# Performance work log

Hardware: AMD Instinct MI355X
Metric: run time of the kernel (lower is better)

## Reference

```python
import jax, jax.numpy as jnp
import numpy as np

BITS = 4
MAXQ = (1 << BITS) - 1      # 15
PACK = 32 // BITS           # 8 values per int32 word
GROUP = 128                 # quantization group size along K


def setup_inputs() -> dict:
    key = jax.random.key(0)
    k0, k1, k2, k3 = jax.random.split(key, 4)
    M, K, N = 4096, 4096, 11008
    G = K // GROUP
    x = jax.random.normal(k0, (M, K), dtype=jnp.float32)
    # packed 4-bit weights: full-range random int32 words (each holds 8 nibbles)
    qweight = jax.random.randint(k1, (K // PACK, N), -(2**31), 2**31 - 1, dtype=jnp.int32)
    # packed zero points: (G, N // PACK) int32 words
    qzeros = jax.random.randint(k2, (G, N // PACK), -(2**31), 2**31 - 1, dtype=jnp.int32)
    # group-wise scales (G, N), small positive values as GPTQ produces
    scales = jax.random.uniform(k3, (G, N), dtype=jnp.float32, minval=1e-3, maxval=1e-2)
    # standard GPTQ grouping: consecutive blocks of GROUP rows share a group
    g_idx = (jnp.arange(K) // GROUP).astype(jnp.int32)
    return {"x": x, "qweight": qweight, "scales": scales, "qzeros": qzeros, "g_idx": g_idx}


def _dequant(qweight, scales, qzeros, g_idx):
    """Unpack int32-packed 4-bit weights and dequantize to float. Returns (K, N)."""
    K = g_idx.shape[0]
    N = qweight.shape[1]
    k = jnp.arange(K)
    # nibble k lives in word k//PACK at bit offset (k%PACK)*BITS
    k_shift = ((k % PACK) * BITS).astype(jnp.int32)
    w = (qweight[k // PACK] >> k_shift[:, None]) & MAXQ              # (K, N) int32 in [0, MAXQ]
    n = jnp.arange(N)
    n_shift = ((n % PACK) * BITS).astype(jnp.int32)
    z = ((qzeros[:, n // PACK] >> n_shift[None, :]) & MAXQ) + 1      # (G, N); kernel adds 1
    return (w - z[g_idx]).astype(scales.dtype) * scales[g_idx]       # (K, N) float


def reference(x, qweight, scales, qzeros, g_idx):
    # C = A @ dequant(B), fp32 accumulation as in the Triton kernel
    W = _dequant(qweight, scales, qzeros, g_idx)
    return jnp.matmul(x, W, preferred_element_type=jnp.float32)
```

## Files before the change

### kernel.cpp

```cpp
#include <hip/hip_runtime.h>
#include <hip/hip_bf16.h>
#include <stdint.h>

typedef _Float16 half8 __attribute__((ext_vector_type(8)));
typedef __attribute__((ext_vector_type(8))) short short8;
typedef __attribute__((ext_vector_type(4))) float floatx4;
typedef __attribute__((ext_vector_type(4))) uint32_t uint32x4;

#define GROUP_SZ 128

__device__ __forceinline__ uint32_t cvt_pk_f16(float lo, float hi) {
    uint32_t r;
    asm("v_cvt_pkrtz_f16_f32 %0, %1, %2" : "=v"(r) : "v"(lo), "v"(hi));
    return r;
}
__device__ __forceinline__ uint32_t pk_add_f16(uint32_t a, uint32_t b) {
    uint32_t r;
    asm("v_pk_add_f16 %0, %1, %2" : "=v"(r) : "v"(a), "v"(b));
    return r;
}
__device__ __forceinline__ uint32_t pk_mul_f16(uint32_t a, uint32_t b) {
    uint32_t r;
    asm("v_pk_mul_f16 %0, %1, %2" : "=v"(r) : "v"(a), "v"(b));
    return r;
}

__global__ __launch_bounds__(256)
void convA_kernel(const float* __restrict__ x, uint4* __restrict__ aws, int total8) {
    int idx = blockIdx.x * 256 + threadIdx.x;
    if (idx >= total8) return;
    const float4* xp = reinterpret_cast<const float4*>(x) + (size_t)idx * 2;
    float4 a = xp[0], b = xp[1];
    uint4 o;
    o.x = cvt_pk_f16(a.x, a.y);
    o.y = cvt_pk_f16(a.z, a.w);
    o.z = cvt_pk_f16(b.x, b.y);
    o.w = cvt_pk_f16(b.z, b.w);
    aws[idx] = o;
}

__global__ __launch_bounds__(256)
void deqB_kernel(const int* __restrict__ qw, const float* __restrict__ sc,
                 const int* __restrict__ qz, char* __restrict__ bws, int K, int N) {
    const int n = blockIdx.x * 256 + threadIdx.x;
    const int wk = blockIdx.y;
    if (n >= N) return;
    const uint32_t w = (uint32_t)qw[(size_t)wk * N + n];
    const int g = wk >> 4;
    const float s = sc[(size_t)g * N + n];
    const uint32_t zw = (uint32_t)qz[(size_t)g * (N >> 3) + (n >> 3)];
    const float zf = -(float)(1025u + ((zw >> ((n & 7) * 4)) & 15u));
    const uint32_t c2 = cvt_pk_f16(zf, zf);
    const uint32_t s2 = cvt_pk_f16(s, s);
    uint32_t oo[4];
    #pragma unroll
    for (int i = 0; i < 4; ++i) {
        const uint32_t tt = w >> (8 * i);
        const uint32_t qi = ((tt & 0xFu) | 0x64006400u) | ((tt << 12) & 0xF0000u);
        oo[i] = pk_mul_f16(pk_add_f16(qi, c2), s2);
    }
    uint4 o; o.x = oo[0]; o.y = oo[1]; o.z = oo[2]; o.w = oo[3];
    const int NKT = K >> 6;
    const int nt = n >> 8, h = (n >> 7) & 1, row = n & 127;
    const int kt = wk >> 3, slot = wk & 7;
    size_t off = ((((size_t)nt * NKT + kt) * 2 + h) * 8 + slot) * 2048 + (size_t)row * 16;
    *reinterpret_cast<uint4*>(bws + off) = o;
}

__global__ __launch_bounds__(512, 2)
void gemm8_kernel(const char* __restrict__ Aws, const char* __restrict__ Bws,
                  float* __restrict__ out, int M, int K, int N) {
    __shared__ char smem[65536];

    const int NT = K >> 6;
    const int nbm = M >> 8, nbn = N >> 8;
    const int nwg = nbm * nbn;
    int bid = blockIdx.x;
    int q = nwg >> 3, r = nwg & 7;
    int xcd = bid & 7, lin = bid >> 3;
    int sid = (xcd < r ? xcd * (q + 1) : r * (q + 1) + (xcd - r) * q) + lin;
    const int bm = sid % nbm, bn = sid / nbm;
    const int m0 = bm << 8, n0 = bn << 8;

    const int tid = threadIdx.x;
    const int lane = tid & 63, w = tid >> 6;
    const int wm = w >> 2, wn = w & 3;
    const int fr = lane & 15, hi = lane >> 4;
    const int r8 = lane >> 3, c8 = lane & 7;

    const uint32_t K2 = (uint32_t)K * 2;
    const char* aBase = Aws + (size_t)m0 * K2;
    uint32_t aOff[2][2];
    #pragma unroll
    for (int h = 0; h < 2; ++h)
        #pragma unroll
        for (int i = 0; i < 2; ++i)
            aOff[h][i] = (uint32_t)(h * 128 + w * 16 + i * 8 + r8) * K2
                       + (uint32_t)((c8 ^ r8) * 16);
    const char* bBase = Bws + (size_t)bn * ((size_t)NT * 32768);

    auto stageA = [&](uint32_t buf, int kt) {
        #pragma unroll
        for (int h = 0; h < 2; ++h)
            #pragma unroll
            for (int i = 0; i < 2; ++i) {
                const char* src = aBase + aOff[h][i] + (uint32_t)kt * 128u;
                char* dst = smem + buf * 32768u + (uint32_t)h * 16384u
                                 + (uint32_t)w * 2048u + (uint32_t)i * 1024u;
                __builtin_amdgcn_global_load_lds(
                    (const __attribute__((address_space(1))) void*)src,
                    (__attribute__((address_space(3))) void*)dst, 16, 0, 0);
            }
    };

    floatx4 acc[8][4];
    const floatx4 fz = {0.f, 0.f, 0.f, 0.f};
    #pragma unroll
    for (int i = 0; i < 8; ++i)
        #pragma unroll
        for (int j = 0; j < 4; ++j) acc[i][j] = fz;
    half8 af_a[4][2], af_b[4][2];
    half8 bf_x[2][2], bf_y[2][2];

#define LOAD_AF(AF, QM) { _Pragma("unroll") for (int fmi = 0; fmi < 4; ++fmi) { \
    _Pragma("unroll") for (int kk = 0; kk < 2; ++kk) { \
        uint32_t row = (uint32_t)(wm * 128 + ((QM) * 4 + fmi) * 16 + fr); \
        uint32_t p = (uint32_t)((kk * 4 + hi) ^ (fr & 7)); \
        uint32x4 u = *reinterpret_cast<const uint32x4*>(As + row * 128u + p * 16u); \
        AF[fmi][kk] = __builtin_bit_cast(half8, u); } } }

#define LOAD_BFG(BF, QN, KT) { _Pragma("unroll") for (int fnj = 0; fnj < 2; ++fnj) { \
    _Pragma("unroll") for (int kk = 0; kk < 2; ++kk) { \
        uint32_t nl = (uint32_t)(wn * 64 + ((QN) * 2 + fnj) * 16 + fr); \
        uint32_t slot = (uint32_t)(kk * 4 + hi); \
        size_t off = ((size_t)((KT) * 2 + (int)(nl >> 7)) * 8 + slot) * 2048 \
                   + (size_t)(nl & 127u) * 16u; \
        uint32x4 u = *reinterpret_cast<const uint32x4*>(bBase + off); \
        BF[fnj][kk] = __builtin_bit_cast(half8, u); } } }

#define MM(AF, BF, QM, QN) { _Pragma("unroll") for (int kk = 0; kk < 2; ++kk) \
    _Pragma("unroll") for (int fmi = 0; fmi < 4; ++fmi) \
    _Pragma("unroll") for (int fnj = 0; fnj < 2; ++fnj) \
        acc[(QM) * 4 + fmi][(QN) * 2 + fnj] = __builtin_amdgcn_mfma_f32_16x16x32_f16( \
            AF[fmi][kk], BF[fnj][kk], acc[(QM) * 4 + fmi][(QN) * 2 + fnj], 0, 0, 0); }

    stageA(0, 0);
    if (NT > 1) stageA(1, 1);
    LOAD_BFG(bf_x, 0, 0);
    LOAD_BFG(bf_y, 1, 0);
    if (NT > 1) { asm volatile("s_waitcnt vmcnt(12)" ::: "memory"); }
    else        { asm volatile("s_waitcnt vmcnt(8)" ::: "memory"); }
    __builtin_amdgcn_s_barrier();

    for (int t = 0; t < NT; ++t) {
        const uint32_t c = (uint32_t)(t & 1);
        const char* As = smem + c * 32768u;
        const bool st1 = (t + 1 < NT);
        const bool st2 = (t + 2 < NT);
        LOAD_AF(af_a, 0);
        LOAD_AF(af_b, 1);
        __builtin_amdgcn_s_setprio(1);
        MM(af_a, bf_x, 0, 0);
        MM(af_b, bf_x, 1, 0);
        __builtin_amdgcn_s_setprio(0);
        if (st1) LOAD_BFG(bf_x, 0, t + 1);
        __builtin_amdgcn_s_setprio(1);
        MM(af_a, bf_y, 0, 1);
        MM(af_b, bf_y, 1, 1);
        __builtin_amdgcn_s_setprio(0);
        if (st1) LOAD_BFG(bf_y, 1, t + 1);
        __builtin_amdgcn_s_barrier();
        if (st2) {
            stageA(c, t + 2);
            asm volatile("s_waitcnt vmcnt(12)" ::: "memory");
        } else if (st1) {
            asm volatile("s_waitcnt vmcnt(8)" ::: "memory");
        }
        if (st1) __builtin_amdgcn_s_barrier();
    }
#undef LOAD_AF
#undef LOAD_BFG
#undef MM

    float* op = out + (size_t)(m0 + wm * 128) * N + n0 + wn * 64;
    #pragma unroll
    for (int fm = 0; fm < 8; ++fm)
        #pragma unroll
        for (int fn = 0; fn < 4; ++fn)
            #pragma unroll
            for (int rr = 0; rr < 4; ++rr)
                op[(size_t)(fm * 16 + hi * 4 + rr) * N + fn * 16 + fr] = acc[fm][fn][rr];
}

__device__ __forceinline__ uint32_t cvt_pk_bf16(float lo, float hi) {
    uint32_t r;
    asm("v_cvt_pk_bf16_f32 %0, %1, %2" : "=v"(r) : "v"(lo), "v"(hi));
    return r;
}
__device__ __forceinline__ uint32_t fswz(uint32_t row, uint32_t byte_in_row) {
    return row * 128u + (byte_in_row ^ ((row & 7u) << 4));
}

__global__ __launch_bounds__(256, 2)
void fused128_kernel(const float* __restrict__ x, const int* __restrict__ qweight,
                     const float* __restrict__ scales, const int* __restrict__ qzeros,
                     float* __restrict__ out, int M, int K, int N) {
    __shared__ char smem[32768];
    char* Ald = smem;
    char* Bld = smem + 16384;
    const int nbm = M / 128, nbn = N / 128;
    const int nwg = nbm * nbn;
    int bid = blockIdx.x;
    int q = nwg >> 3, r = nwg & 7;
    int xcd = bid & 7, lin = bid >> 3;
    int sid = (xcd < r ? xcd * (q + 1) : r * (q + 1) + (xcd - r) * q) + lin;
    int bm = sid / nbn, bn = sid % nbn;
    const int m0 = bm * 128, n0 = bn * 128;
    const int t = threadIdx.x;
    const int lane = t & 63, wave = t >> 6;
    const int tm = t >> 4, tk4 = t & 15;
    const int sn = t & 127, kwh = t >> 7;
    const int gn = n0 + sn;
    const int NT = K / 64;
    float4 av[8]; uint32_t qw[4]; float sc; uint32_t zw;
    const float* xp = x + (size_t)(m0 + tm) * K + tk4 * 4;
    const int* qp = qweight + (size_t)(kwh * 4) * N + gn;
    auto load_tile = [&](int ts) {
        const int k0 = ts * 64;
        #pragma unroll
        for (int i = 0; i < 8; ++i)
            av[i] = *reinterpret_cast<const float4*>(xp + (size_t)i * 16 * K + k0);
        const int g = k0 >> 7;
        sc = scales[(size_t)g * N + gn];
        zw = (uint32_t)qzeros[(size_t)g * (N >> 3) + (gn >> 3)];
        const int* qb = qp + (size_t)(k0 >> 3) * N;
        #pragma unroll
        for (int j = 0; j < 4; ++j) qw[j] = (uint32_t)qb[(size_t)j * N];
    };
    const int zsh = (gn & 7) * 4;
    auto write_tile = [&]() {
        #pragma unroll
        for (int i = 0; i < 8; ++i) {
            uint2 p;
            p.x = cvt_pk_bf16(av[i].x, av[i].y);
            p.y = cvt_pk_bf16(av[i].z, av[i].w);
            *reinterpret_cast<uint2*>(Ald + fswz((uint32_t)(i * 16 + tm), (uint32_t)(tk4 * 8))) = p;
        }
        const float z = (float)((zw >> zsh) & 15u) + 1.0f;
        const float nz = -z * sc;
        #pragma unroll
        for (int j = 0; j < 4; ++j) {
            const uint32_t wv = qw[j];
            float f[8];
            #pragma unroll
            for (int e = 0; e < 8; ++e)
                f[e] = fmaf((float)((wv >> (4 * e)) & 15u), sc, nz);
            uint4 p;
            p.x = cvt_pk_bf16(f[0], f[1]); p.y = cvt_pk_bf16(f[2], f[3]);
            p.z = cvt_pk_bf16(f[4], f[5]); p.w = cvt_pk_bf16(f[6], f[7]);
            *reinterpret_cast<uint4*>(Bld + fswz((uint32_t)sn, (uint32_t)((kwh * 4 + j) * 16))) = p;
        }
    };
    floatx4 acc[4][4];
    const floatx4 fz = {0.f, 0.f, 0.f, 0.f};
    #pragma unroll
    for (int i = 0; i < 4; ++i)
        #pragma unroll
        for (int j = 0; j < 4; ++j) acc[i][j] = fz;
    const int wm = (wave >> 1) * 64, wn = (wave & 1) * 64;
    const int fr = lane & 15;
    const int fkb = ((lane >> 4) * 8) * 2;
    auto compute = [&]() {
        #pragma unroll
        for (int kk = 0; kk < 2; ++kk) {
            short8 afv[4], bfv[4];
            #pragma unroll
            for (int i = 0; i < 4; ++i)
                afv[i] = *reinterpret_cast<const short8*>(
                    Ald + fswz((uint32_t)(wm + i * 16 + fr), (uint32_t)(kk * 64 + fkb)));
            #pragma unroll
            for (int i = 0; i < 4; ++i)
                bfv[i] = *reinterpret_cast<const short8*>(
                    Bld + fswz((uint32_t)(wn + i * 16 + fr), (uint32_t)(kk * 64 + fkb)));
            #pragma unroll
            for (int i = 0; i < 4; ++i)
                #pragma unroll
                for (int j = 0; j < 4; ++j)
                    acc[i][j] = __builtin_amdgcn_mfma_f32_16x16x32_bf16(afv[i], bfv[j], acc[i][j], 0, 0, 0);
        }
    };
    load_tile(0);
    write_tile();
    __syncthreads();
    for (int ts = 0; ts < NT; ++ts) {
        if (ts + 1 < NT) load_tile(ts + 1);
        compute();
        __syncthreads();
        if (ts + 1 < NT) write_tile();
        __syncthreads();
    }
    const int fq = lane >> 4;
    float* op = out + (size_t)(m0 + wm) * N + n0 + wn;
    #pragma unroll
    for (int i = 0; i < 4; ++i)
        #pragma unroll
        for (int j = 0; j < 4; ++j)
            #pragma unroll
            for (int rr = 0; rr < 4; ++rr)
                op[(size_t)(i * 16 + fq * 4 + rr) * N + j * 16 + fr] = acc[i][j][rr];
}

extern "C" void kernel_launch(void* const* d_in, const int* in_sizes, int n_in,
                              void* d_out, int out_size, void* d_ws, size_t ws_size,
                              hipStream_t stream) {
    const float* x       = (const float*)d_in[0];
    const int*   qweight = (const int*)d_in[1];
    const float* scales  = (const float*)d_in[2];
    const int*   qzeros  = (const int*)d_in[3];

    const int K = in_sizes[4];
    const int M = in_sizes[0] / K;
    const int G = K / GROUP_SZ;
    const int N = in_sizes[2] / G;
    float* out = (float*)d_out;

    const size_t needA = (size_t)M * K * 2;
    const size_t needB = (size_t)K * (size_t)N * 2;
    const bool ok = (ws_size >= needA + needB) && (M % 256 == 0) && (N % 256 == 0)
                    && (K % 128 == 0) && (N % 8 == 0);
    if (ok) {
        char* aws = (char*)d_ws;
        char* bws = aws + needA;
        const int total8 = M * (K / 8);
        hipLaunchKernelGGL(convA_kernel, dim3((total8 + 255) / 256), dim3(256), 0, stream,
                           x, (uint4*)aws, total8);
        hipLaunchKernelGGL(deqB_kernel, dim3((N + 255) / 256, K / 8), dim3(256), 0, stream,
                           qweight, scales, qzeros, bws, K, N);
        hipLaunchKernelGGL(gemm8_kernel, dim3((M / 256) * (N / 256)), dim3(512), 0, stream,
                           aws, bws, out, M, K, N);
    } else {
        const int nwg = (M / 128) * (N / 128);
        hipLaunchKernelGGL(fused128_kernel, dim3(nwg), dim3(256), 0, stream,
                           x, qweight, scales, qzeros, out, M, K, N);
    }
}
```

Before: 388.0 us.

## Pre-tile A into MFMA fragment layout and load operands directly to registers

The A conversion kernel now writes fp16 activations in a tiled layout matching the 16x32 MFMA fragment order, so each lane can fetch its fragment with one contiguous 16-byte global load. The GEMM drops LDS staging, async global-to-LDS copies and all barriers, and instead double-buffers A and B fragments in registers straight from global memory. This removes LDS traffic and synchronisation. The cost is that A reuse across the four N-waves now relies on L2/L1 cache rather than shared memory, which raises global load volume and register pressure.

```diff
diff --git a/kernel.cpp b/kernel.cpp
--- a/kernel.cpp
+++ b/kernel.cpp
@@ -26,17 +26,23 @@
 }
 
 __global__ __launch_bounds__(256)
-void convA_kernel(const float* __restrict__ x, uint4* __restrict__ aws, int total8) {
+void convA_kernel(const float* __restrict__ x, char* __restrict__ aws,
+                  int M, int K) {
+    const int KC = K >> 3;
     int idx = blockIdx.x * 256 + threadIdx.x;
-    if (idx >= total8) return;
-    const float4* xp = reinterpret_cast<const float4*>(x) + (size_t)idx * 2;
+    if (idx >= M * KC) return;
+    const int m = idx / KC, c = idx % KC;
+    const float4* xp = reinterpret_cast<const float4*>(x + (size_t)m * K + c * 8);
     float4 a = xp[0], b = xp[1];
     uint4 o;
     o.x = cvt_pk_f16(a.x, a.y);
     o.y = cvt_pk_f16(a.z, a.w);
     o.z = cvt_pk_f16(b.x, b.y);
     o.w = cvt_pk_f16(b.z, b.w);
-    aws[idx] = o;
+    const int kt = c >> 3, slot = c & 7;
+    size_t off = (((size_t)(m >> 4) * (size_t)(K >> 6) + (size_t)kt) * 8 + (size_t)slot) * 256
+               + (size_t)(m & 15) * 16;
+    *reinterpret_cast<uint4*>(aws + off) = o;
 }
 
 __global__ __launch_bounds__(256)
@@ -68,10 +74,8 @@
 }
 
 __global__ __launch_bounds__(512, 2)
-void gemm8_kernel(const char* __restrict__ Aws, const char* __restrict__ Bws,
-                  float* __restrict__ out, int M, int K, int N) {
-    __shared__ char smem[65536];
-
+void gemmrr_kernel(const char* __restrict__ Aws, const char* __restrict__ Bws,
+                   float* __restrict__ out, int M, int K, int N) {
     const int NT = K >> 6;
     const int nbm = M >> 8, nbn = N >> 8;
     const int nwg = nbm * nbn;
@@ -83,35 +87,21 @@
     const int m0 = bm << 8, n0 = bn << 8;
 
     const int tid = threadIdx.x;
-    const int lane = tid & 63, w = tid >> 6;
-    const int wm = w >> 2, wn = w & 3;
+    const int lane = tid & 63;
+    const int wu = __builtin_amdgcn_readfirstlane(tid >> 6);
+    const int wm = wu >> 2, wn = wu & 3;
     const int fr = lane & 15, hi = lane >> 4;
-    const int r8 = lane >> 3, c8 = lane & 7;
-
-    const uint32_t K2 = (uint32_t)K * 2;
-    const char* aBase = Aws + (size_t)m0 * K2;
-    uint32_t aOff[2][2];
-    #pragma unroll
-    for (int h = 0; h < 2; ++h)
-        #pragma unroll
-        for (int i = 0; i < 2; ++i)
-            aOff[h][i] = (uint32_t)(h * 128 + w * 16 + i * 8 + r8) * K2
-                       + (uint32_t)((c8 ^ r8) * 16);
-    const char* bBase = Bws + (size_t)bn * ((size_t)NT * 32768);
-
-    auto stageA = [&](uint32_t buf, int kt) {
-        #pragma unroll
-        for (int h = 0; h < 2; ++h)
-            #pragma unroll
-            for (int i = 0; i < 2; ++i) {
-                const char* src = aBase + aOff[h][i] + (uint32_t)kt * 128u;
-                char* dst = smem + buf * 32768u + (uint32_t)h * 16384u
-                                 + (uint32_t)w * 2048u + (uint32_t)i * 1024u;
-                __builtin_amdgcn_global_load_lds(
-                    (const __attribute__((address_space(1))) void*)src,
-                    (__attribute__((address_space(3))) void*)dst, 16, 0, 0);
-            }
-    };
+
+    size_t aB[8];
+    #pragma unroll
+    for (int fm = 0; fm < 8; ++fm)
+        aB[fm] = (size_t)((m0 >> 4) + wm * 8 + fm) * (size_t)NT * 2048;
+    uint32_t aOff = 0;
+    const uint32_t aLane = (uint32_t)lane * 16u;
+
+    size_t bU = (size_t)bn * ((size_t)NT * 32768)
+              + (size_t)((wn >> 1) * 16384 + (wn & 1) * 1024);
+    const uint32_t bLane = (uint32_t)hi * 2048u + (uint32_t)fr * 16u;
 
     floatx4 acc[8][4];
     const floatx4 fz = {0.f, 0.f, 0.f, 0.f};
@@ -119,67 +109,36 @@
     for (int i = 0; i < 8; ++i)
         #pragma unroll
         for (int j = 0; j < 4; ++j) acc[i][j] = fz;
-    half8 af_a[4][2], af_b[4][2];
-    half8 bf_x[2][2], bf_y[2][2];
-
-#define LOAD_AF(AF, QM) { _Pragma("unroll") for (int fmi = 0; fmi < 4; ++fmi) { \
-    _Pragma("unroll") for (int kk = 0; kk < 2; ++kk) { \
-        uint32_t row = (uint32_t)(wm * 128 + ((QM) * 4 + fmi) * 16 + fr); \
-        uint32_t p = (uint32_t)((kk * 4 + hi) ^ (fr & 7)); \
-        uint32x4 u = *reinterpret_cast<const uint32x4*>(As + row * 128u + p * 16u); \
-        AF[fmi][kk] = __builtin_bit_cast(half8, u); } } }
-
-#define LOAD_BFG(BF, QN, KT) { _Pragma("unroll") for (int fnj = 0; fnj < 2; ++fnj) { \
-    _Pragma("unroll") for (int kk = 0; kk < 2; ++kk) { \
-        uint32_t nl = (uint32_t)(wn * 64 + ((QN) * 2 + fnj) * 16 + fr); \
-        uint32_t slot = (uint32_t)(kk * 4 + hi); \
-        size_t off = ((size_t)((KT) * 2 + (int)(nl >> 7)) * 8 + slot) * 2048 \
-                   + (size_t)(nl & 127u) * 16u; \
-        uint32x4 u = *reinterpret_cast<const uint32x4*>(bBase + off); \
-        BF[fnj][kk] = __builtin_bit_cast(half8, u); } } }
-
-#define MM(AF, BF, QM, QN) { _Pragma("unroll") for (int kk = 0; kk < 2; ++kk) \
-    _Pragma("unroll") for (int fmi = 0; fmi < 4; ++fmi) \
-    _Pragma("unroll") for (int fnj = 0; fnj < 2; ++fnj) \
-        acc[(QM) * 4 + fmi][(QN) * 2 + fnj] = __builtin_amdgcn_mfma_f32_16x16x32_f16( \
-            AF[fmi][kk], BF[fnj][kk], acc[(QM) * 4 + fmi][(QN) * 2 + fnj], 0, 0, 0); }
-
-    stageA(0, 0);
-    if (NT > 1) stageA(1, 1);
-    LOAD_BFG(bf_x, 0, 0);
-    LOAD_BFG(bf_y, 1, 0);
-    if (NT > 1) { asm volatile("s_waitcnt vmcnt(12)" ::: "memory"); }
-    else        { asm volatile("s_waitcnt vmcnt(8)" ::: "memory"); }
-    __builtin_amdgcn_s_barrier();
+    half8 afA[8], afB[8];
+    half8 bfA[4], bfB[4];
+
+#define LD8(DST, ADDR) { uint32x4 u = *reinterpret_cast<const uint32x4*>(ADDR); \
+    DST = __builtin_bit_cast(half8, u); }
+
+#define LOAD_A(AF, EXTRA) { _Pragma("unroll") for (int fm = 0; fm < 8; ++fm) \
+    LD8(AF[fm], Aws + aB[fm] + aOff + (EXTRA) + aLane) }
+
+#define LOAD_B(BF, EXTRA) { _Pragma("unroll") for (int fn = 0; fn < 4; ++fn) \
+    LD8(BF[fn], Bws + bU + (EXTRA) + (uint32_t)(fn * 256) + bLane) }
+
+#define MM(AF, BF) { _Pragma("unroll") for (int fm = 0; fm < 8; ++fm) \
+    _Pragma("unroll") for (int fn = 0; fn < 4; ++fn) \
+        acc[fm][fn] = __builtin_amdgcn_mfma_f32_16x16x32_f16( \
+            AF[fm], BF[fn], acc[fm][fn], 0, 0, 0); }
+
+    LOAD_A(afA, 0u); LOAD_B(bfA, 0u);
 
     for (int t = 0; t < NT; ++t) {
-        const uint32_t c = (uint32_t)(t & 1);
-        const char* As = smem + c * 32768u;
-        const bool st1 = (t + 1 < NT);
-        const bool st2 = (t + 2 < NT);
-        LOAD_AF(af_a, 0);
-        LOAD_AF(af_b, 1);
-        __builtin_amdgcn_s_setprio(1);
-        MM(af_a, bf_x, 0, 0);
-        MM(af_b, bf_x, 1, 0);
-        __builtin_amdgcn_s_setprio(0);
-        if (st1) LOAD_BFG(bf_x, 0, t + 1);
-        __builtin_amdgcn_s_setprio(1);
-        MM(af_a, bf_y, 0, 1);
-        MM(af_b, bf_y, 1, 1);
-        __builtin_amdgcn_s_setprio(0);
-        if (st1) LOAD_BFG(bf_y, 1, t + 1);
-        __builtin_amdgcn_s_barrier();
-        if (st2) {
-            stageA(c, t + 2);
-            asm volatile("s_waitcnt vmcnt(12)" ::: "memory");
-        } else if (st1) {
-            asm volatile("s_waitcnt vmcnt(8)" ::: "memory");
-        }
-        if (st1) __builtin_amdgcn_s_barrier();
+        LOAD_A(afB, 1024u); LOAD_B(bfB, 8192u);
+        __builtin_amdgcn_s_setprio(1); MM(afA, bfA); __builtin_amdgcn_s_setprio(0);
+        if (t + 1 < NT) { LOAD_A(afA, 2048u); LOAD_B(bfA, 32768u); }
+        __builtin_amdgcn_s_setprio(1); MM(afB, bfB); __builtin_amdgcn_s_setprio(0);
+        aOff += 2048u;
+        bU += 32768u;
     }
-#undef LOAD_AF
-#undef LOAD_BFG
+#undef LD8
+#undef LOAD_A
+#undef LOAD_B
 #undef MM
 
     float* op = out + (size_t)(m0 + wm * 128) * N + n0 + wn * 64;
@@ -331,12 +290,12 @@
     if (ok) {
         char* aws = (char*)d_ws;
         char* bws = aws + needA;
-        const int total8 = M * (K / 8);
-        hipLaunchKernelGGL(convA_kernel, dim3((total8 + 255) / 256), dim3(256), 0, stream,
-                           x, (uint4*)aws, total8);
+        const int totalA = M * (K / 8);
+        hipLaunchKernelGGL(convA_kernel, dim3((totalA + 255) / 256), dim3(256), 0, stream,
+                           x, aws, M, K);
         hipLaunchKernelGGL(deqB_kernel, dim3((N + 255) / 256, K / 8), dim3(256), 0, stream,
                            qweight, scales, qzeros, bws, K, N);
-        hipLaunchKernelGGL(gemm8_kernel, dim3((M / 256) * (N / 256)), dim3(512), 0, stream,
+        hipLaunchKernelGGL(gemmrr_kernel, dim3((M / 256) * (N / 256)), dim3(512), 0, stream,
                            aws, bws, out, M, K, N);
     } else {
         const int nwg = (M / 128) * (N / 128);
```

Result: slower. 456.8 us (+17.7%).
